# Kernel tuning notes

Hardware: AMD Instinct MI355X
Metric: run time of the kernel (lower is better)

The kernel has to match this reference:

```python
import jax, jax.numpy as jnp
import numpy as np

EPS = 1e-06
K = 256  # output_num_tokens


def setup_inputs() -> dict:
    key = jax.random.key(0)
    k1, k2, k3 = jax.random.split(key, 3)
    b, h, n, d = 8, 12, 1024, 64
    attn = jax.random.uniform(k1, (b, h, n, n), dtype=jnp.float32)
    attn = attn / attn.sum(-1, keepdims=True)  # attention probabilities
    value = jax.random.normal(k2, (b, h, n, d), dtype=jnp.float32)
    mask = jnp.ones((b, n), dtype=bool)
    # gumbel noise for the K samples over the n-1 non-cls tokens (torch draws this inside forward)
    u = jax.random.uniform(k3, (b, K, n - 1), dtype=jnp.float32)
    gumbel = -jnp.log(-jnp.log(u + EPS) + EPS)
    return {"attn": attn, "value": value, "mask": mask, "gumbel": gumbel}


def reference(attn, value, mask, gumbel):
    b, h, n, _ = attn.shape
    # cls-token attention to all other tokens, weighted by value norms
    cls_attn = attn[..., 0, 1:]                              # [b, h, n-1]
    value_norms = jnp.linalg.norm(value[..., 1:, :], axis=-1)  # [b, h, n-1]
    cls_attn = jnp.einsum('bhn,bhn->bn', cls_attn, value_norms)
    normed = cls_attn / (cls_attn.sum(-1, keepdims=True) + EPS)
    logits = jnp.log(normed + EPS)                           # [b, n-1]
    mask_value = -jnp.finfo(attn.dtype).max / 2
    logits = jnp.where(mask[:, 1:], logits, mask_value)
    # gumbel top-k sampling: K independent argmax draws (ids offset by 1 for cls)
    sampled = jnp.argmax(logits[:, None, :] + gumbel, axis=-1) + 1  # [b, K]
    # sorted unique with 0-padding at the end (fixed-width version of torch.unique+pad_sequence)
    s = jnp.sort(sampled, axis=-1)
    dup = jnp.concatenate([jnp.zeros((b, 1), bool), s[:, 1:] == s[:, :-1]], axis=1)
    BIG = n + 1
    s = jnp.sort(jnp.where(dup, BIG, s), axis=-1)
    uniq = jnp.where(s == BIG, 0, s)                         # [b, K], zeros pad tail
    new_mask = uniq != 0
    # prepend cls token (id 0, always kept)
    uniq = jnp.pad(uniq, ((0, 0), (1, 0)))                   # [b, K+1]
    new_mask = jnp.pad(new_mask, ((0, 0), (1, 0)), constant_values=True)
    # gather selected rows of attn: [b, h, K+1, n]
    idx = jnp.broadcast_to(uniq[:, None, :, None], (b, h, K + 1, n))
    new_attn = jnp.take_along_axis(attn, idx, axis=2)
    return new_attn, new_mask, uniq
```

## Files before the change

### kernel.cpp

```cpp
#include <hip/hip_runtime.h>
#include <math.h>

#define B   8
#define H   12
#define N   1024
#define D   64
#define KS  256
#define NM1 1023
#define EPSF 1e-6f
#define BIGV 1025

__global__ void k_normw(const float* __restrict__ value,
                        const float* __restrict__ attn,
                        float* __restrict__ p) {
    int gwave = (blockIdx.x * blockDim.x + threadIdx.x) >> 6;
    int lane  = threadIdx.x & 63;
    const int total = B * H * NM1;
    if (gwave >= total) return;
    int bh = gwave / NM1;
    int j  = gwave % NM1;
    float v = value[((size_t)bh * N + j + 1) * D + lane];
    v *= v;
    #pragma unroll
    for (int off = 32; off > 0; off >>= 1) v += __shfl_down(v, off);
    if (lane == 0) {
        float a0 = attn[(size_t)bh * N * N + 1 + j];
        p[bh * NM1 + j] = a0 * sqrtf(v);
    }
}

__global__ void k_logits(const float* __restrict__ p,
                         float* __restrict__ logits) {
    int b   = blockIdx.x;
    int tid = threadIdx.x;
    __shared__ float red[1024];

    float w = 0.f;
    if (tid < NM1) {
        #pragma unroll
        for (int h = 0; h < H; ++h)
            w += p[(b * H + h) * NM1 + tid];
    }
    red[tid] = w;
    __syncthreads();
    for (int s = 512; s > 0; s >>= 1) {
        if (tid < s) red[tid] += red[tid + s];
        __syncthreads();
    }
    float S = red[0];
    if (tid < NM1)
        logits[b * NM1 + tid] = logf(w / (S + EPSF) + EPSF);
}

__global__ void k_argmax(const float* __restrict__ logits,
                         const float* __restrict__ gumbel,
                         int* __restrict__ sampled) {
    int blk = blockIdx.x;
    int b   = blk >> 8;
    int k   = blk & 255;
    int tid = threadIdx.x;
    __shared__ float sv[256];
    __shared__ int   si[256];

    const float* lg = logits + b * NM1;
    const float* gm = gumbel + (size_t)(b * KS + k) * NM1;

    float best = -INFINITY;
    int   bj   = NM1;
    for (int j = tid; j < NM1; j += 256) {
        float v = lg[j] + gm[j];
        if (v > best) { best = v; bj = j; }
    }
    sv[tid] = best;
    si[tid] = bj;
    __syncthreads();
    for (int s = 128; s > 0; s >>= 1) {
        if (tid < s) {
            float v2 = sv[tid + s];
            int   j2 = si[tid + s];
            if (v2 > sv[tid] || (v2 == sv[tid] && j2 < si[tid])) {
                sv[tid] = v2; si[tid] = j2;
            }
        }
        __syncthreads();
    }
    if (tid == 0) sampled[b * KS + k] = si[0] + 1;
}

__device__ __forceinline__ void bitonic256(int* s, int tid) {
    for (int k2 = 2; k2 <= KS; k2 <<= 1) {
        for (int j = k2 >> 1; j > 0; j >>= 1) {
            int ixj = tid ^ j;
            if (ixj > tid) {
                int a = s[tid], c = s[ixj];
                bool up = ((tid & k2) == 0);
                if ((a > c) == up) { s[tid] = c; s[ixj] = a; }
            }
            __syncthreads();
        }
    }
}

__global__ void k_sortdedup(const int* __restrict__ sampled,
                            int* __restrict__ uniq,
                            float* __restrict__ out_mask,
                            float* __restrict__ out_uniq) {
    int b   = blockIdx.x;
    int tid = threadIdx.x;
    __shared__ int s[KS];

    s[tid] = sampled[b * KS + tid];
    __syncthreads();
    bitonic256(s, tid);

    int v   = s[tid];
    int dup = (tid > 0 && v == s[tid - 1]) ? 1 : 0;
    __syncthreads();
    s[tid] = dup ? BIGV : v;
    __syncthreads();
    bitonic256(s, tid);

    int u = (s[tid] == BIGV) ? 0 : s[tid];
    int base = b * (KS + 1);
    uniq[base + 1 + tid]     = u;
    out_uniq[base + 1 + tid] = (float)u;
    out_mask[base + 1 + tid] = (u != 0) ? 1.0f : 0.0f;
    if (tid == 0) {
        uniq[base]     = 0;
        out_uniq[base] = 0.0f;
        out_mask[base] = 1.0f;
    }
}

__global__ void k_gather(const float* __restrict__ attn,
                         const int* __restrict__ uniq,
                         float* __restrict__ out) {
    int blk = blockIdx.x;
    int k   = blk % (KS + 1);
    int bh  = blk / (KS + 1);
    int b   = bh / H;
    int row = uniq[b * (KS + 1) + k];
    const float4* src = (const float4*)(attn + ((size_t)bh * N + row) * N);
    float4*       dst = (float4*)(out + (size_t)blk * N);
    dst[threadIdx.x] = src[threadIdx.x];
}

extern "C" void kernel_launch(void* const* d_in, const int* in_sizes, int n_in,
                              void* d_out, int out_size, void* d_ws, size_t ws_size,
                              hipStream_t stream) {
    const float* attn   = (const float*)d_in[0];
    const float* value  = (const float*)d_in[1];
    const float* gumbel = (const float*)d_in[3];

    float* out      = (float*)d_out;
    float* out_attn = out;
    float* out_mask = out + (size_t)B * H * (KS + 1) * N;
    float* out_uniq = out_mask + B * (KS + 1);

    float* p       = (float*)d_ws;
    float* logits  = p + B * H * NM1;
    int*   sampled = (int*)(logits + B * NM1);
    int*   uniq    = sampled + B * KS;

    const int totalw = B * H * NM1;
    const int nb1 = (totalw * 64 + 255) / 256;
    k_normw<<<nb1, 256, 0, stream>>>(value, attn, p);
    k_logits<<<B, 1024, 0, stream>>>(p, logits);
    k_argmax<<<B * KS, 256, 0, stream>>>(logits, gumbel, sampled);
    k_sortdedup<<<B, 256, 0, stream>>>(sampled, uniq, out_mask, out_uniq);
    k_gather<<<B * H * (KS + 1), 256, 0, stream>>>(attn, uniq, out_attn);
}
```

Measured before the change: 536.4 us.

## Replace sort-based dedup with atomic bitmask and fuse head-sum into norm kernel

Each wavefront in the norm kernel now sums value-norm-weighted cls attention over all heads, so the per-head intermediate and the separate logits kernel go away. The argmax kernel uses one wavefront per sample: it recomputes the normalizer and the log on the fly, reduces with shuffles and records the sampled id by atomically setting a bit in a per-batch bitmask. A small finalize kernel turns the bitmask into sorted unique ids with popcount prefix sums, replacing two bitonic sorts. This removes kernel launches and block-level syncs, at the cost of redundant normalizer sums and logf calls in every argmax wave. The bitmask is zeroed inside the norm kernel, which relies on stream ordering.

```diff
diff --git a/kernel.cpp b/kernel.cpp
--- a/kernel.cpp
+++ b/kernel.cpp
@@ -8,124 +8,102 @@
 #define KS  256
 #define NM1 1023
 #define EPSF 1e-6f
-#define BIGV 1025
 
 __global__ void k_normw(const float* __restrict__ value,
                         const float* __restrict__ attn,
-                        float* __restrict__ p) {
-    int gwave = (blockIdx.x * blockDim.x + threadIdx.x) >> 6;
-    int lane  = threadIdx.x & 63;
-    const int total = B * H * NM1;
-    if (gwave >= total) return;
-    int bh = gwave / NM1;
-    int j  = gwave % NM1;
-    float v = value[((size_t)bh * N + j + 1) * D + lane];
-    v *= v;
+                        float* __restrict__ w,
+                        unsigned int* __restrict__ bitmask) {
+    if (blockIdx.x == 0 && threadIdx.x < B * 32)
+        bitmask[threadIdx.x] = 0u;
+
+    int wid  = (blockIdx.x * blockDim.x + threadIdx.x) >> 6;
+    int lane = threadIdx.x & 63;
+    if (wid >= B * NM1) return;
+    int b = wid / NM1;
+    int j = wid % NM1;
+
+    float wsum = 0.f;
+    for (int h = 0; h < H; ++h) {
+        int bh = b * H + h;
+        float v = value[((size_t)bh * N + j + 1) * D + lane];
+        v *= v;
+        #pragma unroll
+        for (int off = 32; off > 0; off >>= 1) v += __shfl_xor(v, off);
+        float a0 = attn[(size_t)bh * N * N + 1 + j];
+        wsum += a0 * sqrtf(v);
+    }
+    if (lane == 0) w[b * NM1 + j] = wsum;
+}
+
+__global__ void k_argmax(const float* __restrict__ w,
+                         const float* __restrict__ gumbel,
+                         unsigned int* __restrict__ bitmask) {
+    int wid  = (blockIdx.x * blockDim.x + threadIdx.x) >> 6;
+    int lane = threadIdx.x & 63;
+    if (wid >= B * KS) return;
+    int b = wid >> 8;
+    int k = wid & 255;
+
+    const float* wrow = w + b * NM1;
+
+    float s = 0.f;
+    for (int j = lane; j < NM1; j += 64) s += wrow[j];
     #pragma unroll
-    for (int off = 32; off > 0; off >>= 1) v += __shfl_down(v, off);
+    for (int off = 32; off > 0; off >>= 1) s += __shfl_xor(s, off);
+    float Sden = s + EPSF;
+
+    const float* gm = gumbel + (size_t)(b * KS + k) * NM1;
+    float best = -INFINITY;
+    int   bj   = NM1;
+    for (int j = lane; j < NM1; j += 64) {
+        float v = logf(wrow[j] / Sden + EPSF) + gm[j];
+        if (v > best) { best = v; bj = j; }
+    }
+    #pragma unroll
+    for (int off = 32; off > 0; off >>= 1) {
+        float v2 = __shfl_xor(best, off);
+        int   j2 = __shfl_xor(bj, off);
+        if (v2 > best || (v2 == best && j2 < bj)) { best = v2; bj = j2; }
+    }
     if (lane == 0) {
-        float a0 = attn[(size_t)bh * N * N + 1 + j];
-        p[bh * NM1 + j] = a0 * sqrtf(v);
+        int sv = bj + 1;
+        atomicOr(&bitmask[b * 32 + (sv >> 5)], 1u << (sv & 31));
     }
 }
 
-__global__ void k_logits(const float* __restrict__ p,
-                         float* __restrict__ logits) {
-    int b   = blockIdx.x;
-    int tid = threadIdx.x;
-    __shared__ float red[1024];
+__global__ void k_finalize(const unsigned int* __restrict__ bitmask,
+                           int* __restrict__ uniq,
+                           float* __restrict__ out_mask,
+                           float* __restrict__ out_uniq) {
+    int b    = blockIdx.x;
+    int lane = threadIdx.x;
+    unsigned int m = (lane < 32) ? bitmask[b * 32 + lane] : 0u;
+    int pc  = __popc(m);
+    int inc = pc;
+    #pragma unroll
+    for (int off = 1; off < 64; off <<= 1) {
+        int nv = __shfl_up(inc, off);
+        if (lane >= off) inc += nv;
+    }
+    int ex    = inc - pc;
+    int total = __shfl(inc, 63);
 
-    float w = 0.f;
-    if (tid < NM1) {
-        #pragma unroll
-        for (int h = 0; h < H; ++h)
-            w += p[(b * H + h) * NM1 + tid];
+    int base = b * (KS + 1);
+    while (m) {
+        int bit = __ffs(m) - 1;
+        m &= m - 1;
+        int val  = lane * 32 + bit;
+        int slot = base + 1 + ex++;
+        uniq[slot]     = val;
+        out_uniq[slot] = (float)val;
+        out_mask[slot] = 1.0f;
     }
-    red[tid] = w;
-    __syncthreads();
-    for (int s = 512; s > 0; s >>= 1) {
-        if (tid < s) red[tid] += red[tid + s];
-        __syncthreads();
+    for (int t = total + lane; t < KS; t += 64) {
+        uniq[base + 1 + t]     = 0;
+        out_uniq[base + 1 + t] = 0.0f;
+        out_mask[base + 1 + t] = 0.0f;
     }
-    float S = red[0];
-    if (tid < NM1)
-        logits[b * NM1 + tid] = logf(w / (S + EPSF) + EPSF);
-}
-
-__global__ void k_argmax(const float* __restrict__ logits,
-                         const float* __restrict__ gumbel,
-                         int* __restrict__ sampled) {
-    int blk = blockIdx.x;
-    int b   = blk >> 8;
-    int k   = blk & 255;
-    int tid = threadIdx.x;
-    __shared__ float sv[256];
-    __shared__ int   si[256];
-
-    const float* lg = logits + b * NM1;
-    const float* gm = gumbel + (size_t)(b * KS + k) * NM1;
-
-    float best = -INFINITY;
-    int   bj   = NM1;
-    for (int j = tid; j < NM1; j += 256) {
-        float v = lg[j] + gm[j];
-        if (v > best) { best = v; bj = j; }
-    }
-    sv[tid] = best;
-    si[tid] = bj;
-    __syncthreads();
-    for (int s = 128; s > 0; s >>= 1) {
-        if (tid < s) {
-            float v2 = sv[tid + s];
-            int   j2 = si[tid + s];
-            if (v2 > sv[tid] || (v2 == sv[tid] && j2 < si[tid])) {
-                sv[tid] = v2; si[tid] = j2;
-            }
-        }
-        __syncthreads();
-    }
-    if (tid == 0) sampled[b * KS + k] = si[0] + 1;
-}
-
-__device__ __forceinline__ void bitonic256(int* s, int tid) {
-    for (int k2 = 2; k2 <= KS; k2 <<= 1) {
-        for (int j = k2 >> 1; j > 0; j >>= 1) {
-            int ixj = tid ^ j;
-            if (ixj > tid) {
-                int a = s[tid], c = s[ixj];
-                bool up = ((tid & k2) == 0);
-                if ((a > c) == up) { s[tid] = c; s[ixj] = a; }
-            }
-            __syncthreads();
-        }
-    }
-}
-
-__global__ void k_sortdedup(const int* __restrict__ sampled,
-                            int* __restrict__ uniq,
-                            float* __restrict__ out_mask,
-                            float* __restrict__ out_uniq) {
-    int b   = blockIdx.x;
-    int tid = threadIdx.x;
-    __shared__ int s[KS];
-
-    s[tid] = sampled[b * KS + tid];
-    __syncthreads();
-    bitonic256(s, tid);
-
-    int v   = s[tid];
-    int dup = (tid > 0 && v == s[tid - 1]) ? 1 : 0;
-    __syncthreads();
-    s[tid] = dup ? BIGV : v;
-    __syncthreads();
-    bitonic256(s, tid);
-
-    int u = (s[tid] == BIGV) ? 0 : s[tid];
-    int base = b * (KS + 1);
-    uniq[base + 1 + tid]     = u;
-    out_uniq[base + 1 + tid] = (float)u;
-    out_mask[base + 1 + tid] = (u != 0) ? 1.0f : 0.0f;
-    if (tid == 0) {
+    if (lane == 0) {
         uniq[base]     = 0;
         out_uniq[base] = 0.0f;
         out_mask[base] = 1.0f;
@@ -157,16 +135,12 @@
     float* out_mask = out + (size_t)B * H * (KS + 1) * N;
     float* out_uniq = out_mask + B * (KS + 1);
 
-    float* p       = (float*)d_ws;
-    float* logits  = p + B * H * NM1;
-    int*   sampled = (int*)(logits + B * NM1);
-    int*   uniq    = sampled + B * KS;
+    float*        w       = (float*)d_ws;
+    unsigned int* bitmask = (unsigned int*)(w + B * NM1);
+    int*          uniq    = (int*)(bitmask + B * 32);
 
-    const int totalw = B * H * NM1;
-    const int nb1 = (totalw * 64 + 255) / 256;
-    k_normw<<<nb1, 256, 0, stream>>>(value, attn, p);
-    k_logits<<<B, 1024, 0, stream>>>(p, logits);
-    k_argmax<<<B * KS, 256, 0, stream>>>(logits, gumbel, sampled);
-    k_sortdedup<<<B, 256, 0, stream>>>(sampled, uniq, out_mask, out_uniq);
+    k_normw<<<(B * NM1) / 4, 256, 0, stream>>>(value, attn, w, bitmask);
+    k_argmax<<<(B * KS) / 4, 256, 0, stream>>>(w, gumbel, bitmask);
+    k_finalize<<<B, 64, 0, stream>>>(bitmask, uniq, out_mask, out_uniq);
     k_gather<<<B * H * (KS + 1), 256, 0, stream>>>(attn, uniq, out_attn);
 }
```

Result: no change. 526.5 us (-1.9%).
